# Optimization experiments

Measured on AMD Instinct MI355X. Metric: run time of the kernel, lower is better.

The kernel has to match this reference:

```python
import jax, jax.numpy as jnp
import numpy as np

NUM_NODES = 100000
IN_DIM = 64
OUT_DIM = 64
NUM_EDGES = 1250000


def setup_inputs() -> dict:
    key = jax.random.key(0)
    k1, k2, k3, k4, k5 = jax.random.split(key, 5)
    x = jax.random.normal(k1, (NUM_NODES, IN_DIM), dtype=jnp.float32)
    edge_index = jax.random.randint(k2, (2, NUM_EDGES), 0, NUM_NODES, dtype=jnp.int32)
    # Linear params (PyTorch default init: uniform(-1/sqrt(in), 1/sqrt(in)))
    bound = 1.0 / np.sqrt(IN_DIM)
    W_self = jax.random.uniform(k3, (OUT_DIM, IN_DIM), minval=-bound, maxval=bound, dtype=jnp.float32)
    b_self = jax.random.uniform(k4, (OUT_DIM,), minval=-bound, maxval=bound, dtype=jnp.float32)
    W_neigh = jax.random.uniform(k5, (OUT_DIM, IN_DIM), minval=-bound, maxval=bound, dtype=jnp.float32)
    return {"x": x, "edge_index": edge_index, "W_self": W_self, "b_self": b_self, "W_neigh": W_neigh}


def reference(x, edge_index, W_self, b_self, W_neigh):
    # x: [N, D_in], edge_index: [2, E]
    src, dst = edge_index[0], edge_index[1]
    num_nodes = x.shape[0]
    x_src = x[src]  # [E, D_in] gather
    neigh_agg = jax.ops.segment_sum(x_src, dst, num_segments=num_nodes)  # [N, D_in]
    deg = jax.ops.segment_sum(jnp.ones_like(dst, dtype=x.dtype), dst, num_segments=num_nodes)
    deg = jnp.clip(deg, 1.0, None)[:, None]
    neigh_mean = neigh_agg / deg
    out = x @ W_self.T + b_self + neigh_mean @ W_neigh.T
    return jax.nn.relu(out)
```

## Files before the change

### kernel.cpp

```cpp
#include <hip/hip_runtime.h>


#define BKSH 9
#define BKN 512
#define NBMAX 256
#define CAPE 7168
#define WPT (CAPE / BKN)
#define CHUNK 4096
#define EPT (CHUNK / 256)

typedef __attribute__((ext_vector_type(8))) short short8;
typedef __attribute__((ext_vector_type(4))) float floatx4;

static __device__ inline unsigned short f2bf(float f) {
  union { float f; unsigned int u; } v;
  v.f = f;
  unsigned int r = v.u + 0x7FFFu + ((v.u >> 16) & 1u);
  return (unsigned short)(r >> 16);
}

static __device__ inline short8 pack8(float4 a, float4 b) {
  short8 s;
  s[0] = (short)f2bf(a.x); s[1] = (short)f2bf(a.y);
  s[2] = (short)f2bf(a.z); s[3] = (short)f2bf(a.w);
  s[4] = (short)f2bf(b.x); s[5] = (short)f2bf(b.y);
  s[6] = (short)f2bf(b.z); s[7] = (short)f2bf(b.w);
  return s;
}

static __device__ inline void add8(float* a, short8 sv) {
  union { short8 s; unsigned int u[4]; } c; c.s = sv;
#pragma unroll
  for (int i = 0; i < 4; ++i) {
    a[2 * i]     += __uint_as_float(c.u[i] << 16);
    a[2 * i + 1] += __uint_as_float(c.u[i] & 0xFFFF0000u);
  }
}

__global__ __launch_bounds__(256) void k1_main(
    const float* __restrict__ x,
    const float* __restrict__ Wself, const float* __restrict__ bself,
    const float* __restrict__ Wneigh,
    float* __restrict__ yb, unsigned short* __restrict__ zb,
    const int* __restrict__ src, const int* __restrict__ dst,
    int* __restrict__ cursor, int* __restrict__ ebuf,
    int E, int N, int NB, int SCB) {
  __shared__ int h[NBMAX], loff[NBMAX], gbase[NBMAX];
  __shared__ int sbuf[CHUNK];
  int t = threadIdx.x;
  int bid = blockIdx.x;

  if (bid >= SCB) {
    int lane = t & 63;
    int w = t >> 6;
    int tb = (bid - SCB) * 64 + w * 16;
    int m = lane & 15, q = lane >> 4;

    long long rowA = (long long)min(tb + m, N - 1) * 64;
    short8 ax[2];
#pragma unroll
    for (int ks = 0; ks < 2; ++ks) {
      const float* xr = &x[rowA + ks * 32 + q * 8];
      ax[ks] = pack8(*(const float4*)xr, *(const float4*)(xr + 4));
    }

#pragma unroll
    for (int nt = 0; nt < 4; ++nt) {
      int ob = nt * 16;
      long long rowB = (long long)(ob + m) * 64;
      floatx4 accs = {0.f, 0.f, 0.f, 0.f};
      floatx4 accn = {0.f, 0.f, 0.f, 0.f};
#pragma unroll
      for (int ks = 0; ks < 2; ++ks) {
        const float* pw = &Wself[rowB + ks * 32 + q * 8];
        short8 bs = pack8(*(const float4*)pw, *(const float4*)(pw + 4));
        accs = __builtin_amdgcn_mfma_f32_16x16x32_bf16(ax[ks], bs, accs, 0, 0, 0);
        const float* pn = &Wneigh[rowB + ks * 32 + q * 8];
        short8 bn = pack8(*(const float4*)pn, *(const float4*)(pn + 4));
        accn = __builtin_amdgcn_mfma_f32_16x16x32_bf16(ax[ks], bn, accn, 0, 0, 0);
      }
      float bias = bself[ob + m];
#pragma unroll
      for (int r = 0; r < 4; ++r) {
        int node = tb + q * 4 + r;
        if (node < N) {
          yb[(long long)node * 64 + ob + m] = accs[r] + bias;
          zb[(long long)node * 64 + ob + m] = f2bf(accn[r]);
        }
      }
    }
    return;
  }

  if (t < NBMAX) h[t] = 0;
  __syncthreads();

  int base = bid * CHUNK;
  int myd[EPT], mys[EPT];
#pragma unroll
  for (int i = 0; i < EPT; ++i) {
    int e = base + t + 256 * i;
    if (e < E) {
      myd[i] = dst[e];
      mys[i] = src[e];
      atomicAdd(&h[myd[i] >> BKSH], 1);
    } else myd[i] = -1;
  }
  __syncthreads();

  if (t < 64) {
    int i0 = 4 * t;
    int v0 = h[i0], v1 = h[i0 + 1], v2 = h[i0 + 2], v3 = h[i0 + 3];
    int s4 = v0 + v1 + v2 + v3, inc = s4;
#pragma unroll
    for (int off = 1; off < 64; off <<= 1) {
      int u = __shfl_up(inc, off, 64);
      if (t >= off) inc += u;
    }
    int ex = inc - s4;
    loff[i0] = ex; loff[i0 + 1] = ex + v0;
    loff[i0 + 2] = ex + v0 + v1; loff[i0 + 3] = ex + v0 + v1 + v2;
  }
  __syncthreads();

  if (t < NB) {
    if (h[t] > 0) gbase[t] = t * CAPE + atomicAdd(&cursor[t], h[t]);
  }
  if (t < NBMAX) h[t] = 0;
  __syncthreads();

#pragma unroll
  for (int i = 0; i < EPT; ++i) {
    if (myd[i] >= 0) {
      int b = myd[i] >> BKSH;
      int p = atomicAdd(&h[b], 1);
      sbuf[loff[b] + p] = mys[i] | ((myd[i] & (BKN - 1)) << 17);
    }
  }
  __syncthreads();

  int w = t >> 6, lane = t & 63;
  for (int b = w; b < NB; b += 4) {
    int c = h[b], lo = loff[b], go = gbase[b];
    for (int j = lane; j < c; j += 64)
      ebuf[go + j] = sbuf[lo + j];
  }
}

__global__ __launch_bounds__(512) void sb_csr(const int* __restrict__ cursor,
                                              const int* __restrict__ ebuf,
                                              int* __restrict__ col,
                                              int2* __restrict__ rowse, int N) {
  __shared__ int sbuf[CAPE];
  __shared__ int cnt[BKN];
  __shared__ int wsum[8];
  int b = blockIdx.x, t = threadIdx.x;
  int s = b * CAPE;
  int n = cursor[b];
  int e = s + n;

  int my[WPT];
#pragma unroll
  for (int i = 0; i < WPT; ++i) {
    int j = s + t + i * BKN;
    my[i] = (j < e) ? ebuf[j] : -1;
  }

  cnt[t] = 0;
  __syncthreads();
#pragma unroll
  for (int i = 0; i < WPT; ++i)
    if (my[i] >= 0) atomicAdd(&cnt[(my[i] >> 17) & (BKN - 1)], 1);
  __syncthreads();

  int v = cnt[t];
  int lane = t & 63, w = t >> 6;
  int inc = v;
#pragma unroll
  for (int o = 1; o < 64; o <<= 1) {
    int u = __shfl_up(inc, o, 64);
    if (lane >= o) inc += u;
  }
  if (lane == 63) wsum[w] = inc;
  __syncthreads();
  if (t < 8) {
    int s0 = wsum[t], incw = s0;
#pragma unroll
    for (int o = 1; o < 8; o <<= 1) {
      int u = __shfl_up(incw, o, 64);
      if (t >= o) incw += u;
    }
    wsum[t] = incw - s0;
  }
  __syncthreads();
  int ex = wsum[w] + inc - v;
  int node = (b << BKSH) + t;
  if (node < N) rowse[node] = make_int2(s + ex, v);
  __syncthreads();
  cnt[t] = ex;
  __syncthreads();

#pragma unroll
  for (int i = 0; i < WPT; ++i) {
    if (my[i] >= 0) {
      int nl = (my[i] >> 17) & (BKN - 1);
      int p = atomicAdd(&cnt[nl], 1);
      sbuf[p] = my[i] & 0x1FFFF;
    }
  }
  __syncthreads();

  for (int j = t; j < n; j += BKN) col[s + j] = sbuf[j];
}

__global__ __launch_bounds__(256) void gather_final(
    const unsigned short* __restrict__ zb,
    const int2* __restrict__ rowse,
    const int* __restrict__ col,
    const float* __restrict__ yb,
    float* __restrict__ out, int N) {
  int gid = blockIdx.x * 256 + threadIdx.x;
  int node = gid >> 6;
  if (node >= N) return;
  int lane = threadIdx.x & 63;
  int o = lane >> 3, d = lane & 7;
  int2 se = rowse[node];
  int s = se.x, c = se.y, e = s + c;

  float a[8] = {0.f, 0.f, 0.f, 0.f, 0.f, 0.f, 0.f, 0.f};
  float b2[8] = {0.f, 0.f, 0.f, 0.f, 0.f, 0.f, 0.f, 0.f};
  for (int j = s + o; j < e; j += 16) {
    int c0 = col[j];
    bool h2 = (j + 8) < e;
    int c1 = h2 ? col[j + 8] : c0;
    short8 v0 = *(const short8*)&zb[(long long)c0 * 64 + d * 8];
    short8 v1 = *(const short8*)&zb[(long long)c1 * 64 + d * 8];
    add8(a, v0);
    if (h2) add8(b2, v1);
  }
#pragma unroll
  for (int k = 0; k < 8; ++k) a[k] += b2[k];

#pragma unroll
  for (int m = 8; m <= 32; m <<= 1) {
#pragma unroll
    for (int k = 0; k < 8; ++k) a[k] += __shfl_xor(a[k], m, 64);
  }

  if (o == 0) {
    float inv = 1.0f / fmaxf((float)c, 1.0f);
    long long ro = (long long)node * 64 + d * 8;
    float4 y0 = *(const float4*)&yb[ro];
    float4 y1 = *(const float4*)&yb[ro + 4];
    float4 r0, r1;
    r0.x = fmaxf(y0.x + a[0] * inv, 0.f);
    r0.y = fmaxf(y0.y + a[1] * inv, 0.f);
    r0.z = fmaxf(y0.z + a[2] * inv, 0.f);
    r0.w = fmaxf(y0.w + a[3] * inv, 0.f);
    r1.x = fmaxf(y1.x + a[4] * inv, 0.f);
    r1.y = fmaxf(y1.y + a[5] * inv, 0.f);
    r1.z = fmaxf(y1.z + a[6] * inv, 0.f);
    r1.w = fmaxf(y1.w + a[7] * inv, 0.f);
    *(float4*)&out[ro] = r0;
    *(float4*)&out[ro + 4] = r1;
  }
}

extern "C" void kernel_launch(void* const* d_in, const int* in_sizes, int n_in,
                              void* d_out, int out_size, void* d_ws, size_t ws_size,
                              hipStream_t stream) {
  const float* x      = (const float*)d_in[0];
  const int*   eidx   = (const int*)d_in[1];
  const float* Wself  = (const float*)d_in[2];
  const float* bself  = (const float*)d_in[3];
  const float* Wneigh = (const float*)d_in[4];
  float* out = (float*)d_out;

  const int N = in_sizes[0] / 64;
  const int E = in_sizes[1] / 2;
  const int* src = eidx;
  const int* dst = eidx + E;
  const int NB = (N + BKN - 1) / BKN;

  float* yb = (float*)d_ws;
  unsigned short* zb = (unsigned short*)(yb + (size_t)N * 64);
  int* cursor = (int*)(zb + (size_t)N * 64);
  int2* rowse = (int2*)(cursor + NBMAX);
  int* ebuf   = (int*)(rowse + N);
  int* col    = ebuf + (size_t)NB * CAPE;

  hipMemsetAsync(cursor, 0, NBMAX * sizeof(int), stream);

  const int SCB = (E + CHUNK - 1) / CHUNK;
  const int GB = (N + 63) / 64;
  k1_main<<<SCB + GB, 256, 0, stream>>>(x, Wself, bself, Wneigh, yb, zb,
                                        src, dst, cursor, ebuf, E, N, NB, SCB);
  sb_csr<<<NB, BKN, 0, stream>>>(cursor, ebuf, col, rowse, N);
  gather_final<<<(int)(((long long)N * 64 + 255) / 256), 256, 0, stream>>>(
      zb, rowse, col, yb, out, N);
}
```

Baseline: 163.0 us.

## Store self term in bf16, widen k1 blocks, shuffle-broadcast column indices in gather

The self-projection output yb is now stored as bf16 instead of fp32, halving its write and read traffic, at some cost in accuracy. k1_main moves to 512-thread blocks, so each scatter block handles 8 edges per thread and each GEMM block covers 128 nodes. gather_final loads up to 64 column indices once per wave and broadcasts them with shuffles, and prefetches the self term before the neighbour loop. It also skips the gather loop entirely for zero-degree nodes.

```diff
diff --git a/kernel.cpp b/kernel.cpp
--- a/kernel.cpp
+++ b/kernel.cpp
@@ -7,7 +7,8 @@
 #define CAPE 7168
 #define WPT (CAPE / BKN)
 #define CHUNK 4096
-#define EPT (CHUNK / 256)
+#define K1T 512
+#define EPT (CHUNK / K1T)
 
 typedef __attribute__((ext_vector_type(8))) short short8;
 typedef __attribute__((ext_vector_type(4))) float floatx4;
@@ -37,11 +38,20 @@
   }
 }
 
-__global__ __launch_bounds__(256) void k1_main(
+static __device__ inline void cvt8(float* a, short8 sv) {
+  union { short8 s; unsigned int u[4]; } c; c.s = sv;
+#pragma unroll
+  for (int i = 0; i < 4; ++i) {
+    a[2 * i]     = __uint_as_float(c.u[i] << 16);
+    a[2 * i + 1] = __uint_as_float(c.u[i] & 0xFFFF0000u);
+  }
+}
+
+__global__ __launch_bounds__(K1T) void k1_main(
     const float* __restrict__ x,
     const float* __restrict__ Wself, const float* __restrict__ bself,
     const float* __restrict__ Wneigh,
-    float* __restrict__ yb, unsigned short* __restrict__ zb,
+    unsigned short* __restrict__ yb, unsigned short* __restrict__ zb,
     const int* __restrict__ src, const int* __restrict__ dst,
     int* __restrict__ cursor, int* __restrict__ ebuf,
     int E, int N, int NB, int SCB) {
@@ -53,7 +63,7 @@
   if (bid >= SCB) {
     int lane = t & 63;
     int w = t >> 6;
-    int tb = (bid - SCB) * 64 + w * 16;
+    int tb = (bid - SCB) * 128 + w * 16;
     int m = lane & 15, q = lane >> 4;
 
     long long rowA = (long long)min(tb + m, N - 1) * 64;
@@ -84,7 +94,7 @@
       for (int r = 0; r < 4; ++r) {
         int node = tb + q * 4 + r;
         if (node < N) {
-          yb[(long long)node * 64 + ob + m] = accs[r] + bias;
+          yb[(long long)node * 64 + ob + m] = f2bf(accs[r] + bias);
           zb[(long long)node * 64 + ob + m] = f2bf(accn[r]);
         }
       }
@@ -92,6 +102,7 @@
     return;
   }
 
+  int w = t >> 6, lane = t & 63;
   if (t < NBMAX) h[t] = 0;
   __syncthreads();
 
@@ -99,7 +110,7 @@
   int myd[EPT], mys[EPT];
 #pragma unroll
   for (int i = 0; i < EPT; ++i) {
-    int e = base + t + 256 * i;
+    int e = base + t + K1T * i;
     if (e < E) {
       myd[i] = dst[e];
       mys[i] = src[e];
@@ -126,6 +137,7 @@
   if (t < NB) {
     if (h[t] > 0) gbase[t] = t * CAPE + atomicAdd(&cursor[t], h[t]);
   }
+  __syncthreads();
   if (t < NBMAX) h[t] = 0;
   __syncthreads();
 
@@ -139,8 +151,7 @@
   }
   __syncthreads();
 
-  int w = t >> 6, lane = t & 63;
-  for (int b = w; b < NB; b += 4) {
+  for (int b = w; b < NB; b += 8) {
     int c = h[b], lo = loff[b], go = gbase[b];
     for (int j = lane; j < c; j += 64)
       ebuf[go + j] = sbuf[lo + j];
@@ -217,7 +228,7 @@
     const unsigned short* __restrict__ zb,
     const int2* __restrict__ rowse,
     const int* __restrict__ col,
-    const float* __restrict__ yb,
+    const unsigned short* __restrict__ yb,
     float* __restrict__ out, int N) {
   int gid = blockIdx.x * 256 + threadIdx.x;
   int node = gid >> 6;
@@ -225,18 +236,40 @@
   int lane = threadIdx.x & 63;
   int o = lane >> 3, d = lane & 7;
   int2 se = rowse[node];
-  int s = se.x, c = se.y, e = s + c;
+  int s = se.x, c = se.y;
+
+  long long ro = (long long)node * 64 + d * 8;
+  short8 yv8;
+  if (o == 0) {
+    yv8 = *(const short8*)&yb[ro];
+  }
 
   float a[8] = {0.f, 0.f, 0.f, 0.f, 0.f, 0.f, 0.f, 0.f};
   float b2[8] = {0.f, 0.f, 0.f, 0.f, 0.f, 0.f, 0.f, 0.f};
-  for (int j = s + o; j < e; j += 16) {
-    int c0 = col[j];
-    bool h2 = (j + 8) < e;
-    int c1 = h2 ? col[j + 8] : c0;
-    short8 v0 = *(const short8*)&zb[(long long)c0 * 64 + d * 8];
-    short8 v1 = *(const short8*)&zb[(long long)c1 * 64 + d * 8];
-    add8(a, v0);
-    if (h2) add8(b2, v1);
+  if (c > 0 && c <= 64) {
+    int colv = col[s + min(lane, c - 1)];
+    for (int kb = 0; kb < c; kb += 16) {
+      int k0 = kb + o;
+      int k1 = k0 + 8;
+      bool p0 = k0 < c, p1 = k1 < c;
+      int c0 = __shfl(colv, p0 ? k0 : 0, 64);
+      int c1 = __shfl(colv, p1 ? k1 : 0, 64);
+      short8 v0 = *(const short8*)&zb[(long long)c0 * 64 + d * 8];
+      short8 v1 = *(const short8*)&zb[(long long)c1 * 64 + d * 8];
+      if (p0) add8(a, v0);
+      if (p1) add8(b2, v1);
+    }
+  } else if (c > 64) {
+    int e = s + c;
+    for (int j = s + o; j < e; j += 16) {
+      int c0 = col[j];
+      bool h2 = (j + 8) < e;
+      int c1 = h2 ? col[j + 8] : c0;
+      short8 v0 = *(const short8*)&zb[(long long)c0 * 64 + d * 8];
+      short8 v1 = *(const short8*)&zb[(long long)c1 * 64 + d * 8];
+      add8(a, v0);
+      if (h2) add8(b2, v1);
+    }
   }
 #pragma unroll
   for (int k = 0; k < 8; ++k) a[k] += b2[k];
@@ -249,18 +282,17 @@
 
   if (o == 0) {
     float inv = 1.0f / fmaxf((float)c, 1.0f);
-    long long ro = (long long)node * 64 + d * 8;
-    float4 y0 = *(const float4*)&yb[ro];
-    float4 y1 = *(const float4*)&yb[ro + 4];
+    float yv[8];
+    cvt8(yv, yv8);
     float4 r0, r1;
-    r0.x = fmaxf(y0.x + a[0] * inv, 0.f);
-    r0.y = fmaxf(y0.y + a[1] * inv, 0.f);
-    r0.z = fmaxf(y0.z + a[2] * inv, 0.f);
-    r0.w = fmaxf(y0.w + a[3] * inv, 0.f);
-    r1.x = fmaxf(y1.x + a[4] * inv, 0.f);
-    r1.y = fmaxf(y1.y + a[5] * inv, 0.f);
-    r1.z = fmaxf(y1.z + a[6] * inv, 0.f);
-    r1.w = fmaxf(y1.w + a[7] * inv, 0.f);
+    r0.x = fmaxf(yv[0] + a[0] * inv, 0.f);
+    r0.y = fmaxf(yv[1] + a[1] * inv, 0.f);
+    r0.z = fmaxf(yv[2] + a[2] * inv, 0.f);
+    r0.w = fmaxf(yv[3] + a[3] * inv, 0.f);
+    r1.x = fmaxf(yv[4] + a[4] * inv, 0.f);
+    r1.y = fmaxf(yv[5] + a[5] * inv, 0.f);
+    r1.z = fmaxf(yv[6] + a[6] * inv, 0.f);
+    r1.w = fmaxf(yv[7] + a[7] * inv, 0.f);
     *(float4*)&out[ro] = r0;
     *(float4*)&out[ro + 4] = r1;
   }
@@ -282,8 +314,8 @@
   const int* dst = eidx + E;
   const int NB = (N + BKN - 1) / BKN;
 
-  float* yb = (float*)d_ws;
-  unsigned short* zb = (unsigned short*)(yb + (size_t)N * 64);
+  unsigned short* yb = (unsigned short*)d_ws;
+  unsigned short* zb = yb + (size_t)N * 64;
   int* cursor = (int*)(zb + (size_t)N * 64);
   int2* rowse = (int2*)(cursor + NBMAX);
   int* ebuf   = (int*)(rowse + N);
@@ -292,8 +324,8 @@
   hipMemsetAsync(cursor, 0, NBMAX * sizeof(int), stream);
 
   const int SCB = (E + CHUNK - 1) / CHUNK;
-  const int GB = (N + 63) / 64;
-  k1_main<<<SCB + GB, 256, 0, stream>>>(x, Wself, bself, Wneigh, yb, zb,
+  const int GB = (N + 127) / 128;
+  k1_main<<<SCB + GB, K1T, 0, stream>>>(x, Wself, bself, Wneigh, yb, zb,
                                         src, dst, cursor, ebuf, E, N, NB, SCB);
   sb_csr<<<NB, BKN, 0, stream>>>(cursor, ebuf, col, rowse, N);
   gather_final<<<(int)(((long long)N * 64 + 255) / 256), 256, 0, stream>>>(
```

Result: no change. 164.6 us (+1.0%).
